# Kernel tuning notes

Hardware: AMD Instinct MI355X
Metric: run time of the kernel (lower is better)

## Reference

```python
import jax, jax.numpy as jnp
import numpy as np

NHEAD = 8
HB, WB = 16, 16  # block_size


def _mha(q, k, v, w_in, b_in, w_out, b_out, nhead):
    # q,k,v: [L, B, C] seq-first, like torch.nn.MultiheadAttention (eval mode, no dropout)
    Lq, B, C = q.shape
    d = C // nhead
    wq, wk, wv = jnp.split(w_in, 3, axis=0)
    bq, bk, bv = jnp.split(b_in, 3)
    qh = (q @ wq.T + bq).reshape(Lq, B, nhead, d).transpose(1, 2, 0, 3)        # [B,H,Lq,d]
    kh = (k @ wk.T + bk).reshape(k.shape[0], B, nhead, d).transpose(1, 2, 0, 3)
    vh = (v @ wv.T + bv).reshape(v.shape[0], B, nhead, d).transpose(1, 2, 0, 3)
    scale = 1.0 / jnp.sqrt(jnp.asarray(d, dtype=qh.dtype))
    scores = jnp.einsum('bhqd,bhkd->bhqk', qh * scale, kh)
    attn = jax.nn.softmax(scores, axis=-1)
    out = jnp.einsum('bhqk,bhkd->bhqd', attn, vh)                               # [B,H,Lq,d]
    out = out.transpose(2, 0, 1, 3).reshape(Lq, B, C)
    return out @ w_out.T + b_out


def setup_inputs() -> dict:
    key = jax.random.key(0)
    ks = jax.random.split(key, 12)
    n, c, t, h, w = 2, 256, 2, 64, 64
    q = jax.random.normal(ks[0], (n, c, t, h, w), dtype=jnp.float32)
    k = jax.random.normal(ks[1], (n, c, t, h, w), dtype=jnp.float32)
    v = jax.random.normal(ks[2], (n, c, t, h, w), dtype=jnp.float32)
    pos = jax.random.normal(ks[3], (n, c, t, h, w), dtype=jnp.float32)
    s = 0.02
    wl_in = jax.random.normal(ks[4], (3 * c, c), dtype=jnp.float32) * s
    bl_in = jnp.zeros((3 * c,), dtype=jnp.float32)
    wl_out = jax.random.normal(ks[5], (c, c), dtype=jnp.float32) * s
    bl_out = jnp.zeros((c,), dtype=jnp.float32)
    ws_in = jax.random.normal(ks[6], (3 * c, c), dtype=jnp.float32) * s
    bs_in = jnp.zeros((3 * c,), dtype=jnp.float32)
    ws_out = jax.random.normal(ks[7], (c, c), dtype=jnp.float32) * s
    bs_out = jnp.zeros((c,), dtype=jnp.float32)
    return {"q": q, "k": k, "v": v, "pos": pos,
            "wl_in": wl_in, "bl_in": bl_in, "wl_out": wl_out, "bl_out": bl_out,
            "ws_in": ws_in, "bs_in": bs_in, "ws_out": ws_out, "bs_out": bs_out}


def reference(q, k, v, pos, wl_in, bl_in, wl_out, bl_out, ws_in, bs_in, ws_out, bs_out):
    n, c, t_q, h, w = q.shape
    t_k = k.shape[2]
    bn_h, bn_w = h // HB, w // WB

    def to_long(x, t):
        # [n,c,t,h,w] -> [t*bn_h*bn_w, n*HB*WB, c]
        x = x.reshape(n, c, t, bn_h, HB, bn_w, WB).transpose(2, 3, 5, 0, 4, 6, 1)
        return x.reshape(t * bn_h * bn_w, n * HB * WB, c)

    ql = to_long(q, t_q)
    kl = to_long(k, t_k)
    vl = to_long(v, t_k)
    pl = to_long(pos, t_q)

    v1 = _mha(ql + pl, kl + pl, vl, wl_in, bl_in, wl_out, bl_out, NHEAD)

    def long_to_short(x):
        # [t*bn_h*bn_w, n*HB*WB, c] -> [t*HB*WB, n*bn_h*bn_w, c]
        x = x.reshape(t_q, bn_h, bn_w, n, HB, WB, c).transpose(0, 4, 5, 3, 1, 2, 6)
        return x.reshape(t_q * HB * WB, n * bn_h * bn_w, c)

    v2 = long_to_short(v1)
    ps = long_to_short(pl)

    out = _mha(v2 + ps, v2 + ps, v2, ws_in, bs_in, ws_out, bs_out, NHEAD)
    out = out.reshape(t_q, HB, WB, n, bn_h, bn_w, c).transpose(3, 6, 0, 4, 1, 5, 2)
    return out.reshape(n, c, t_q, h, w)
```

## Files before the change

### kernel.cpp

```cpp
#include <hip/hip_runtime.h>
#include <math.h>


#define SCALE_D32 0.17677669529663687f
#define EXP2_SCALE 0.25508680987930193f
#define GLOBAL_AS __attribute__((address_space(1)))
#define LDS_AS __attribute__((address_space(3)))

typedef short short8 __attribute__((ext_vector_type(8)));
typedef short short4v __attribute__((ext_vector_type(4)));
typedef short short2v __attribute__((ext_vector_type(2)));
typedef float floatx4 __attribute__((ext_vector_type(4)));

__device__ __forceinline__ short f2bf(float f) {
  union { float f; unsigned u; } x;
  x.f = f;
  unsigned r = x.u + 0x7fffu + ((x.u >> 16) & 1u);
  return (short)(r >> 16);
}
__device__ __forceinline__ float bf2f(short s) {
  union { unsigned u; float f; } x;
  x.u = ((unsigned)(unsigned short)s) << 16;
  return x.f;
}

__device__ __forceinline__ int o1s_phys(int q, int ch) {
  return q * 256 + (ch & ~63) + ((((ch >> 3) & 7) ^ (q & 7)) << 3) + (ch & 7);
}

__device__ __forceinline__ void stage_w(short* Wsl, const short* Wg, int kb,
                                        int wave, int lane, int rsub, int csub) {
#pragma unroll
  for (int j = 0; j < 8; ++j) {
    int r0 = (wave * 8 + j) * 8;
    int row = r0 + rsub;
    int c = csub ^ (row & 7);
    const short* gp = Wg + (long)row * 256 + kb * 64 + c * 8;
    short* lp = &Wsl[r0 * 64 + lane * 8];
    __builtin_amdgcn_global_load_lds((const GLOBAL_AS void*)gp,
                                     (LDS_AS void*)lp, 16, 0, 0);
  }
}

__device__ __forceinline__ void gemm_direct(
    const short* A, const short* Wg, floatx4 (&acc)[2][4],
    int wave, int l15, int quad, int x7) {
  const short* wrow = Wg + (wave * 64 + l15) * 256 + quad * 8;
  short8 bcur[4], bnxt[4];
#pragma unroll
  for (int nt = 0; nt < 4; ++nt)
    bcur[nt] = *(const short8*)(wrow + nt * 16 * 256);
#pragma unroll
  for (int t = 0; t < 8; ++t) {
    if (t < 7) {
#pragma unroll
      for (int nt = 0; nt < 4; ++nt)
        bnxt[nt] = *(const short8*)(wrow + nt * 16 * 256 + (t + 1) * 32);
    }
    int pcA = ((t & 1) * 4 + quad) ^ x7;
    short8 af[2];
#pragma unroll
    for (int mt = 0; mt < 2; ++mt)
      af[mt] = *(const short8*)&A[(mt * 16 + l15) * 256 + (t >> 1) * 64 + pcA * 8];
#pragma unroll
    for (int mt = 0; mt < 2; ++mt)
#pragma unroll
      for (int nt = 0; nt < 4; ++nt)
        acc[mt][nt] = __builtin_amdgcn_mfma_f32_16x16x32_bf16(
            af[mt], bcur[nt], acc[mt][nt], 0, 0, 0);
    if (t < 7) {
#pragma unroll
      for (int nt = 0; nt < 4; ++nt) bcur[nt] = bnxt[nt];
    }
  }
}

__device__ __forceinline__ void stage_tile(short* dst, const short* Xg,
                                           int b1, int tid) {
#pragma unroll
  for (int p = 0; p < 4; ++p) {
    int idx = p * 256 + tid;
    int row = idx >> 5;
    int ch = idx & 31;
    int chs = (ch & ~7) | ((ch & 7) ^ (row & 7));
    const short* gp = Xg + ((long)(row * 512 + b1)) * 256 + chs * 8;
    short* lp = dst + idx * 8;
    __builtin_amdgcn_global_load_lds((const GLOBAL_AS void*)gp,
                                     (LDS_AS void*)lp, 16, 0, 0);
  }
}

__global__ __launch_bounds__(256) void pack_kernel(
    const float* __restrict__ q, const float* __restrict__ k,
    const float* __restrict__ v, const float* __restrict__ pos,
    short* __restrict__ Xp, short* __restrict__ Xq,
    short* __restrict__ Xk, short* __restrict__ Xv,
    const float* __restrict__ wl_in, const float* __restrict__ wl_out,
    const float* __restrict__ ws_in, const float* __restrict__ ws_out,
    short* __restrict__ wbf) {
  __shared__ float tP[64][65];
  __shared__ float tX[64][65];
  int b = blockIdx.x;
  int cb = b & 3;
  int h  = (b >> 2) & 63;
  int nt = b >> 8;
  int n = nt >> 1, t = nt & 1;
  int c0 = cb * 64;
  int bh = h >> 4, ii = h & 15;
  long inbase = (long)n * 2097152 + (long)t * 4096 + (long)h * 64;
  int tx = threadIdx.x & 63;
  int ty = threadIdx.x >> 6;

  for (int cc = ty; cc < 64; cc += 4) {
    long a = inbase + (long)(c0 + cc) * 8192 + tx;
    tP[cc][tx] = pos[a];
    tX[cc][tx] = q[a];
  }
  __syncthreads();
  for (int ww = ty; ww < 64; ww += 4) {
    int bw = ww >> 4, j = ww & 15;
    int m1 = (((t * 4 + bh) * 4 + bw) * 512) + n * 256 + ii * 16 + j;
    long o = (long)m1 * 256 + c0 + tx;
    float pv = tP[tx][ww];
    Xp[o] = f2bf(pv);
    Xq[o] = f2bf(tX[tx][ww] + pv);
  }
  __syncthreads();
  for (int cc = ty; cc < 64; cc += 4) {
    long a = inbase + (long)(c0 + cc) * 8192 + tx;
    tX[cc][tx] = k[a];
  }
  __syncthreads();
  for (int ww = ty; ww < 64; ww += 4) {
    int bw = ww >> 4, j = ww & 15;
    int m1 = (((t * 4 + bh) * 4 + bw) * 512) + n * 256 + ii * 16 + j;
    long o = (long)m1 * 256 + c0 + tx;
    Xk[o] = f2bf(tX[tx][ww] + tP[tx][ww]);
  }
  __syncthreads();
  for (int cc = ty; cc < 64; cc += 4) {
    long a = inbase + (long)(c0 + cc) * 8192 + tx;
    tX[cc][tx] = v[a];
  }
  __syncthreads();
  for (int ww = ty; ww < 64; ww += 4) {
    int bw = ww >> 4, j = ww & 15;
    int m1 = (((t * 4 + bh) * 4 + bw) * 512) + n * 256 + ii * 16 + j;
    long o = (long)m1 * 256 + c0 + tx;
    Xv[o] = f2bf(tX[tx][ww]);
  }
  int idx = (blockIdx.x * 256 + threadIdx.x) * 2;
  const float* wp;
  if (idx < 196608) wp = wl_in + idx;
  else if (idx < 262144) wp = wl_out + (idx - 196608);
  else if (idx < 458752) wp = ws_in + (idx - 262144);
  else wp = ws_out + (idx - 458752);
  float2 wv = *(const float2*)wp;
  wbf[idx] = f2bf(wv.x);
  wbf[idx + 1] = f2bf(wv.y);
}

template <bool OUT32>
__global__ __launch_bounds__(256) void gemm_tri(
    const short* __restrict__ A0, const short* __restrict__ A1,
    const short* __restrict__ A2, const short* __restrict__ W0,
    const float* __restrict__ bias0, void* __restrict__ C0,
    void* __restrict__ C1, void* __restrict__ C2) {
  __shared__ short As[128 * 64];
  __shared__ short Ws[64 * 64];
  int z = blockIdx.z;
  const short* A = (z == 0) ? A0 : ((z == 1) ? A1 : A2);
  const short* Wb = W0 + z * 65536;
  const float* bias = bias0 + z * 256;
  void* Csel = (z == 0) ? C0 : ((z == 1) ? C1 : C2);
  int m0 = blockIdx.x * 128;
  int n0 = blockIdx.y * 64;
  int tid = threadIdx.x;
  int lane = tid & 63, wave = tid >> 6;
  int wm = wave >> 1, wn = wave & 1;
  int l15 = lane & 15, quad = lane >> 4;
  int x7 = l15 & 7;
  int rsub = lane >> 3;
  int csub = lane & 7;

  floatx4 acc[4][2];
#pragma unroll
  for (int mt = 0; mt < 4; ++mt)
#pragma unroll
    for (int nt = 0; nt < 2; ++nt) acc[mt][nt] = (floatx4)(0.f);

  for (int kb = 0; kb < 4; ++kb) {
    int k0 = kb * 64;
    if (kb) __syncthreads();
#pragma unroll
    for (int j = 0; j < 4; ++j) {
      int r0 = (wave * 4 + j) * 8;
      int row = r0 + rsub;
      int c = csub ^ (row & 7);
      const short* gp = A + (long)(m0 + row) * 256 + k0 + c * 8;
      short* lp = &As[r0 * 64 + lane * 8];
      __builtin_amdgcn_global_load_lds((const GLOBAL_AS void*)gp,
                                       (LDS_AS void*)lp, 16, 0, 0);
    }
#pragma unroll
    for (int j = 0; j < 2; ++j) {
      int r0 = (wave * 2 + j) * 8;
      int row = r0 + rsub;
      int c = csub ^ (row & 7);
      const short* gp = Wb + (long)(n0 + row) * 256 + k0 + c * 8;
      short* lp = &Ws[r0 * 64 + lane * 8];
      __builtin_amdgcn_global_load_lds((const GLOBAL_AS void*)gp,
                                       (LDS_AS void*)lp, 16, 0, 0);
    }
    __syncthreads();
#pragma unroll
    for (int ks = 0; ks < 2; ++ks) {
      int pc = (ks * 4 + quad) ^ x7;
      short8 af[4], bfr[2];
#pragma unroll
      for (int mt = 0; mt < 4; ++mt) {
        int row = wm * 64 + mt * 16 + l15;
        af[mt] = *(const short8*)&As[row * 64 + pc * 8];
      }
#pragma unroll
      for (int nt = 0; nt < 2; ++nt) {
        int row = wn * 32 + nt * 16 + l15;
        bfr[nt] = *(const short8*)&Ws[row * 64 + pc * 8];
      }
#pragma unroll
      for (int mt = 0; mt < 4; ++mt)
#pragma unroll
        for (int nt = 0; nt < 2; ++nt)
          acc[mt][nt] = __builtin_amdgcn_mfma_f32_16x16x32_bf16(
              af[mt], bfr[nt], acc[mt][nt], 0, 0, 0);
    }
  }
  float bia0 = bias[n0 + wn * 32 + l15];
  float bia1 = bias[n0 + wn * 32 + 16 + l15];
#pragma unroll
  for (int mt = 0; mt < 4; ++mt) {
#pragma unroll
    for (int r = 0; r < 4; ++r) {
      int row = m0 + wm * 64 + mt * 16 + quad * 4 + r;
      long base = (long)row * 256 + n0 + wn * 32 + l15;
      if (OUT32) {
        float* C = (float*)Csel;
        C[base] = acc[mt][0][r] + bia0;
        C[base + 16] = acc[mt][1][r] + bia1;
      } else {
        short* C = (short*)Csel;
        C[base] = f2bf(acc[mt][0][r] + bia0);
        C[base + 16] = f2bf(acc[mt][1][r] + bia1);
      }
    }
  }
}

__global__ __launch_bounds__(256) void attn1_giga(
    const short* __restrict__ Xq, const short* __restrict__ Xk,
    const short* __restrict__ Xv, const short* __restrict__ Xp,
    const short* __restrict__ Wlin, const float* __restrict__ bias_lin,
    const short* __restrict__ Wo, const float* __restrict__ bias_o,
    const short* __restrict__ Wsin, const float* __restrict__ bias_sin,
    short* __restrict__ Q2, short* __restrict__ K2, short* __restrict__ V2) {
  __shared__ short R1[32 * 256];
  __shared__ short R2[32 * 256];
  __shared__ short R3[32 * 256];
  __shared__ short R4[10240];
  int b1 = blockIdx.x;
  int tid = threadIdx.x;
  int wave = tid >> 6, lane = tid & 63;
  int l15 = lane & 15, quad = lane >> 4;
  int x7 = l15 & 7;

  stage_tile(R1, Xq, b1, tid);
  stage_tile(R2, Xk, b1, tid);
  stage_tile(R3, Xv, b1, tid);
  __syncthreads();

  floatx4 acc[2][4];

#pragma unroll 1
  for (int z = 0; z < 3; ++z) {
    short* Rz = (z == 0) ? R1 : ((z == 1) ? R2 : R3);
    const short* Wz = Wlin + z * 65536;
#pragma unroll
    for (int mt = 0; mt < 2; ++mt)
#pragma unroll
      for (int nt = 0; nt < 4; ++nt) acc[mt][nt] = (floatx4)(0.f);
    gemm_direct(Rz, Wz, acc, wave, l15, quad, x7);
    __syncthreads();
    float bz[4];
#pragma unroll
    for (int nt = 0; nt < 4; ++nt)
      bz[nt] = bias_lin[z * 256 + wave * 64 + nt * 16 + l15];
#pragma unroll
    for (int mt = 0; mt < 2; ++mt)
#pragma unroll
      for (int r = 0; r < 4; ++r) {
        int row = mt * 16 + quad * 4 + r;
#pragma unroll
        for (int nt = 0; nt < 4; ++nt) {
          int col = wave * 64 + nt * 16 + l15;
          Rz[o1s_phys(row, col)] = f2bf(acc[mt][nt][r] + bz[nt]);
        }
      }
  }
  __syncthreads();

  short* Vtb = R4;
  short* Pwb = R4 + 5120;
  int key = lane & 31;
  int dh = (lane >> 5) * 16;
  int pc2 = 2 * (key & 15) + (key >> 4);

  floatx4 oacc[2][4];
  float lsum[2][2][4];

#pragma unroll
  for (int h2 = 0; h2 < 2; ++h2) {
    int hh = wave * 2 + h2;
    int cb0 = hh * 32 + quad * 8;
    short8 qf0 = *(const short8*)&R1[o1s_phys(l15, cb0)];
    short8 qf1 = *(const short8*)&R1[o1s_phys(l15 + 16, cb0)];
    short8 kf0 = *(const short8*)&R2[o1s_phys(l15, cb0)];
    short8 kf1 = *(const short8*)&R2[o1s_phys(l15 + 16, cb0)];
    short8 v0 = *(const short8*)&R3[o1s_phys(key, hh * 32 + dh)];
    short8 v1 = *(const short8*)&R3[o1s_phys(key, hh * 32 + dh + 8)];
#pragma unroll
    for (int j = 0; j < 8; ++j) {
      Vtb[(wave * 32 + dh + j) * 40 + pc2] = v0[j];
      Vtb[(wave * 32 + dh + 8 + j) * 40 + pc2] = v1[j];
    }
    floatx4 s00 = __builtin_amdgcn_mfma_f32_16x16x32_bf16(qf0, kf0, (floatx4)(0.f), 0, 0, 0);
    floatx4 s01 = __builtin_amdgcn_mfma_f32_16x16x32_bf16(qf0, kf1, (floatx4)(0.f), 0, 0, 0);
    floatx4 s10 = __builtin_amdgcn_mfma_f32_16x16x32_bf16(qf1, kf0, (floatx4)(0.f), 0, 0, 0);
    floatx4 s11 = __builtin_amdgcn_mfma_f32_16x16x32_bf16(qf1, kf1, (floatx4)(0.f), 0, 0, 0);
    float li0[4], li1[4];
#pragma unroll
    for (int r = 0; r < 4; ++r) {
      float p00 = __builtin_amdgcn_exp2f(s00[r] * EXP2_SCALE);
      float p01 = __builtin_amdgcn_exp2f(s01[r] * EXP2_SCALE);
      float p10 = __builtin_amdgcn_exp2f(s10[r] * EXP2_SCALE);
      float p11 = __builtin_amdgcn_exp2f(s11[r] * EXP2_SCALE);
      li0[r] = p00 + p01;
      li1[r] = p10 + p11;
      short2v pa, pb;
      pa.x = f2bf(p00); pa.y = f2bf(p01);
      pb.x = f2bf(p10); pb.y = f2bf(p11);
      *(short2v*)&Pwb[(wave * 32 + quad * 4 + r) * 40 + 2 * l15] = pa;
      *(short2v*)&Pwb[(wave * 32 + 16 + quad * 4 + r) * 40 + 2 * l15] = pb;
    }
#pragma unroll
    for (int r = 0; r < 4; ++r) {
      li0[r] += __shfl_xor(li0[r], 1, 64);
      li0[r] += __shfl_xor(li0[r], 2, 64);
      li0[r] += __shfl_xor(li0[r], 4, 64);
      li0[r] += __shfl_xor(li0[r], 8, 64);
      li1[r] += __shfl_xor(li1[r], 1, 64);
      li1[r] += __shfl_xor(li1[r], 2, 64);
      li1[r] += __shfl_xor(li1[r], 4, 64);
      li1[r] += __shfl_xor(li1[r], 8, 64);
      lsum[h2][0][r] = li0[r];
      lsum[h2][1][r] = li1[r];
    }
    short8 pf0 = *(const short8*)&Pwb[(wave * 32 + l15) * 40 + quad * 8];
    short8 pf1 = *(const short8*)&Pwb[(wave * 32 + 16 + l15) * 40 + quad * 8];
    short8 vt0 = *(const short8*)&Vtb[(wave * 32 + l15) * 40 + quad * 8];
    short8 vt1 = *(const short8*)&Vtb[(wave * 32 + 16 + l15) * 40 + quad * 8];
    oacc[h2][0] = __builtin_amdgcn_mfma_f32_16x16x32_bf16(pf0, vt0, (floatx4)(0.f), 0, 0, 0);
    oacc[h2][1] = __builtin_amdgcn_mfma_f32_16x16x32_bf16(pf0, vt1, (floatx4)(0.f), 0, 0, 0);
    oacc[h2][2] = __builtin_amdgcn_mfma_f32_16x16x32_bf16(pf1, vt0, (floatx4)(0.f), 0, 0, 0);
    oacc[h2][3] = __builtin_amdgcn_mfma_f32_16x16x32_bf16(pf1, vt1, (floatx4)(0.f), 0, 0, 0);
  }

  __syncthreads();

#pragma unroll
  for (int h2 = 0; h2 < 2; ++h2) {
    int hh = wave * 2 + h2;
    int cA = hh * 32 + l15;
    int cB = cA + 16;
#pragma unroll
    for (int r = 0; r < 4; ++r) {
      float inv0 = 1.f / lsum[h2][0][r];
      float inv1 = 1.f / lsum[h2][1][r];
      int qa = quad * 4 + r, qb = 16 + quad * 4 + r;
      R1[o1s_phys(qa, cA)] = f2bf(oacc[h2][0][r] * inv0);
      R1[o1s_phys(qa, cB)] = f2bf(oacc[h2][1][r] * inv0);
      R1[o1s_phys(qb, cA)] = f2bf(oacc[h2][2][r] * inv1);
      R1[o1s_phys(qb, cB)] = f2bf(oacc[h2][3][r] * inv1);
    }
  }
  __syncthreads();

#pragma unroll
  for (int mt = 0; mt < 2; ++mt)
#pragma unroll
    for (int nt = 0; nt < 4; ++nt) acc[mt][nt] = (floatx4)(0.f);
  gemm_direct(R1, Wo, acc, wave, l15, quad, x7);

  {
    float bvo[4];
#pragma unroll
    for (int nt = 0; nt < 4; ++nt) bvo[nt] = bias_o[wave * 64 + nt * 16 + l15];
#pragma unroll
    for (int mt = 0; mt < 2; ++mt) {
#pragma unroll
      for (int r = 0; r < 4; ++r) {
        int qrow = mt * 16 + quad * 4 + r;
        long pbase = ((long)qrow * 512 + b1) * 256;
#pragma unroll
        for (int nt = 0; nt < 4; ++nt) {
          int col = wave * 64 + nt * 16 + l15;
          float val = acc[mt][nt][r] + bvo[nt];
          int ph = o1s_phys(qrow, col);
          R3[ph] = f2bf(val);
          R2[ph] = f2bf(val + bf2f(Xp[pbase + col]));
        }
      }
    }
  }
  __syncthreads();

  int nn = b1 >> 8, ii = (b1 >> 4) & 15, jj = b1 & 15;
#pragma unroll 1
  for (int z = 0; z < 3; ++z) {
    const short* Wz = Wsin + z * 65536;
    const short* Ab = (z < 2) ? R2 : R3;
    short* outz = (z == 0) ? Q2 : ((z == 1) ? K2 : V2);
    float bz[4];
#pragma unroll
    for (int nt = 0; nt < 4; ++nt)
      bz[nt] = bias_sin[z * 256 + wave * 64 + nt * 16 + l15];
#pragma unroll
    for (int mt = 0; mt < 2; ++mt)
#pragma unroll
      for (int nt = 0; nt < 4; ++nt) acc[mt][nt] = (floatx4)(0.f);
    gemm_direct(Ab, Wz, acc, wave, l15, quad, x7);
#pragma unroll
    for (int mt = 0; mt < 2; ++mt) {
#pragma unroll
      for (int r = 0; r < 4; ++r) {
        int qrow = mt * 16 + quad * 4 + r;
        int t = qrow >> 4, bh = (qrow >> 2) & 3, bw = qrow & 3;
        int m2 = (t * 256 + ii * 16 + jj) * 32 + nn * 16 + bh * 4 + bw;
        long xbase = (long)m2 * 256;
#pragma unroll
        for (int nt = 0; nt < 4; ++nt) {
          int col = wave * 64 + nt * 16 + l15;
          outz[xbase + col] = f2bf(acc[mt][nt][r] + bz[nt]);
        }
      }
    }
  }
}

__global__ __launch_bounds__(256) void attn2_mfma(
    const short* __restrict__ Q2, const short* __restrict__ K2,
    const short* __restrict__ V2, short* __restrict__ O2) {
  __shared__ short Ks[64][40];
  __shared__ short Vt[32][72];
  __shared__ short Pw[4][16][72];
  int bid = blockIdx.x;
  int rest = bid & 255;
  int qblk = bid >> 8;
  int hh = 2 * (rest & 3) + (rest >> 7);
  int b2 = (rest >> 2) & 31;
  int tid = threadIdx.x;
  int wave = tid >> 6, lane = tid & 63;
  int l15 = lane & 15, quad = lane >> 4;

  short8 qf;
  {
    long tok = (long)(qblk * 64 + wave * 16 + l15) * 32 + b2;
    qf = *(const short8*)(Q2 + tok * 256 + hh * 32 + quad * 8);
  }
  floatx4 Oa = (floatx4)(0.f), Ob = (floatx4)(0.f);
  float li[4] = {0.f, 0.f, 0.f, 0.f};

  int skey = tid >> 2;
  int sd0 = (tid & 3) * 8;
  int vkey = lane;
  int vd0 = wave * 8;
  int vcol = (vkey & 15) * 4 + (vkey >> 4);

  for (int kb = 0; kb < 8; ++kb) {
    if (kb) __syncthreads();
    {
      long tok = (long)(kb * 64 + skey) * 32 + b2;
      *(short8*)&Ks[skey][sd0] = *(const short8*)(K2 + tok * 256 + hh * 32 + sd0);
    }
    {
      long tok = (long)(kb * 64 + vkey) * 32 + b2;
      short8 v = *(const short8*)(V2 + tok * 256 + hh * 32 + vd0);
#pragma unroll
      for (int j = 0; j < 8; ++j) Vt[vd0 + j][vcol] = v[j];
    }
    __syncthreads();
    floatx4 st[4];
#pragma unroll
    for (int kt = 0; kt < 4; ++kt) {
      short8 kf = *(const short8*)&Ks[kt * 16 + l15][quad * 8];
      st[kt] = __builtin_amdgcn_mfma_f32_16x16x32_bf16(qf, kf, (floatx4)(0.f), 0, 0, 0);
    }
#pragma unroll
    for (int r = 0; r < 4; ++r) {
      float p0 = __builtin_amdgcn_exp2f(st[0][r] * EXP2_SCALE);
      float p1 = __builtin_amdgcn_exp2f(st[1][r] * EXP2_SCALE);
      float p2 = __builtin_amdgcn_exp2f(st[2][r] * EXP2_SCALE);
      float p3 = __builtin_amdgcn_exp2f(st[3][r] * EXP2_SCALE);
      li[r] += (p0 + p1) + (p2 + p3);
      short4v pp;
      pp.x = f2bf(p0); pp.y = f2bf(p1); pp.z = f2bf(p2); pp.w = f2bf(p3);
      *(short4v*)&Pw[wave][quad * 4 + r][l15 * 4] = pp;
    }
#pragma unroll
    for (int kk = 0; kk < 2; ++kk) {
      short8 pf = *(const short8*)&Pw[wave][l15][kk * 32 + quad * 8];
      short8 v0 = *(const short8*)&Vt[l15][kk * 32 + quad * 8];
      short8 v1 = *(const short8*)&Vt[16 + l15][kk * 32 + quad * 8];
      Oa = __builtin_amdgcn_mfma_f32_16x16x32_bf16(pf, v0, Oa, 0, 0, 0);
      Ob = __builtin_amdgcn_mfma_f32_16x16x32_bf16(pf, v1, Ob, 0, 0, 0);
    }
  }
#pragma unroll
  for (int r = 0; r < 4; ++r) {
    float s = li[r];
    s += __shfl_xor(s, 1, 64);
    s += __shfl_xor(s, 2, 64);
    s += __shfl_xor(s, 4, 64);
    s += __shfl_xor(s, 8, 64);
    float inv = 1.f / s;
    long tok = (long)(qblk * 64 + wave * 16 + quad * 4 + r) * 32 + b2;
    long a = tok * 256 + hh * 32 + l15;
    O2[a] = f2bf(Oa[r] * inv);
    O2[a + 16] = f2bf(Ob[r] * inv);
  }
}

__global__ __launch_bounds__(256) void unpack_kernel(
    const float* __restrict__ Y, float* __restrict__ out) {
  __shared__ float tl[64][65];
  int b = blockIdx.x;
  int cb = b & 3;
  int h = (b >> 2) & 63;
  int nt = b >> 8;
  int n = nt >> 1, t = nt & 1;
  int c0 = cb * 64;
  int bh = h >> 4, ii = h & 15;
  int tx = threadIdx.x & 63;
  int ty = threadIdx.x >> 6;
  for (int ww = ty; ww < 64; ww += 4) {
    int bw = ww >> 4, j = ww & 15;
    int l2 = t * 256 + ii * 16 + j;
    int b2 = n * 16 + bh * 4 + bw;
    int m2 = l2 * 32 + b2;
    tl[tx][ww] = Y[(long)m2 * 256 + c0 + tx];
  }
  __syncthreads();
  long ob = (long)n * 2097152 + (long)t * 4096 + (long)h * 64 + tx;
  for (int cc = ty; cc < 64; cc += 4) {
    out[ob + (long)(c0 + cc) * 8192] = tl[cc][tx];
  }
}

extern "C" void kernel_launch(void* const* d_in, const int* in_sizes, int n_in,
                              void* d_out, int out_size, void* d_ws, size_t ws_size,
                              hipStream_t stream) {
  const float* q      = (const float*)d_in[0];
  const float* k      = (const float*)d_in[1];
  const float* v      = (const float*)d_in[2];
  const float* pos    = (const float*)d_in[3];
  const float* wl_in  = (const float*)d_in[4];
  const float* bl_in  = (const float*)d_in[5];
  const float* wl_out = (const float*)d_in[6];
  const float* bl_out = (const float*)d_in[7];
  const float* ws_in  = (const float*)d_in[8];
  const float* bs_in  = (const float*)d_in[9];
  const float* ws_out = (const float*)d_in[10];
  const float* bs_out = (const float*)d_in[11];
  float* out = (float*)d_out;
  char* wsb = (char*)d_ws;
  const size_t SLB = 16777216;
  short* s0 = (short*)(wsb);
  short* wbf = (short*)(wsb + SLB / 2);
  short* s1 = (short*)(wsb + SLB);
  short* s2 = (short*)(wsb + 2 * SLB);
  short* s3 = (short*)(wsb + 3 * SLB);
  short* s4 = (short*)(wsb + 4 * SLB);
  short* s5 = (short*)(wsb + 5 * SLB);
  short* s6 = (short*)(wsb + 6 * SLB);

  pack_kernel<<<1024, 256, 0, stream>>>(q, k, v, pos, s0, s1, s2, s3,
                                        wl_in, wl_out, ws_in, ws_out, wbf);

  attn1_giga<<<512, 256, 0, stream>>>(s1, s2, s3, s0, wbf, bl_in,
                                      wbf + 196608, bl_out,
                                      wbf + 262144, bs_in, s4, s5, s6);

  attn2_mfma<<<2048, 256, 0, stream>>>(s4, s5, s6, s1);
  dim3 g1(128, 4, 1);
  gemm_tri<true><<<g1, 256, 0, stream>>>(s1, s1, s1, wbf + 458752, bs_out,
                                         s2, s2, s2);

  unpack_kernel<<<1024, 256, 0, stream>>>((const float*)s2, out);
}
```

Baseline: 223.4 us.

## Pair two attention tiles per block and share weight slabs through LDS

The fused attention/projection kernel now runs 512 threads handling two 32-row tiles per block. The 256x256 weight matrices are staged into LDS in 64-column slabs and shared by both groups, instead of each wave reading weights directly from global memory. This halves global weight traffic per tile and removes some barriers. In exchange it adds a sync pair per K-slab, uses more LDS (which lowers occupancy), and cuts the grid to 256 blocks. Several __syncthreads were dropped where the new gemm's internal barriers now order the phases.

```diff
diff --git a/kernel.cpp b/kernel.cpp
--- a/kernel.cpp
+++ b/kernel.cpp
@@ -28,65 +28,44 @@
   return q * 256 + (ch & ~63) + ((((ch >> 3) & 7) ^ (q & 7)) << 3) + (ch & 7);
 }
 
-__device__ __forceinline__ void stage_w(short* Wsl, const short* Wg, int kb,
-                                        int wave, int lane, int rsub, int csub) {
-#pragma unroll
-  for (int j = 0; j < 8; ++j) {
-    int r0 = (wave * 8 + j) * 8;
-    int row = r0 + rsub;
-    int c = csub ^ (row & 7);
-    const short* gp = Wg + (long)row * 256 + kb * 64 + c * 8;
-    short* lp = &Wsl[r0 * 64 + lane * 8];
+__device__ __forceinline__ void stage_w512(short* Ws, const short* Wg,
+                                           int kb, int tid) {
+#pragma unroll
+  for (int j = 0; j < 4; ++j) {
+    int idx = j * 512 + tid;
+    int row = idx >> 3;
+    int c = idx & 7;
+    int cs = c ^ (row & 7);
+    const short* gp = Wg + (long)row * 256 + kb * 64 + cs * 8;
     __builtin_amdgcn_global_load_lds((const GLOBAL_AS void*)gp,
-                                     (LDS_AS void*)lp, 16, 0, 0);
-  }
-}
-
-__device__ __forceinline__ void gemm_direct(
-    const short* A, const short* Wg, floatx4 (&acc)[2][4],
-    int wave, int l15, int quad, int x7) {
-  const short* wrow = Wg + (wave * 64 + l15) * 256 + quad * 8;
-  short8 bcur[4], bnxt[4];
-#pragma unroll
-  for (int nt = 0; nt < 4; ++nt)
-    bcur[nt] = *(const short8*)(wrow + nt * 16 * 256);
-#pragma unroll
-  for (int t = 0; t < 8; ++t) {
-    if (t < 7) {
+                                     (LDS_AS void*)(Ws + idx * 8), 16, 0, 0);
+  }
+}
+
+__device__ __forceinline__ void gemm_shared(
+    const short* A, const short* Wg, short* Ws, floatx4 (&acc)[2][4],
+    int tid, int wv, int l15, int quad, int x7) {
+  for (int kb = 0; kb < 4; ++kb) {
+    __syncthreads();
+    stage_w512(Ws, Wg, kb, tid);
+    __syncthreads();
+#pragma unroll
+    for (int ks = 0; ks < 2; ++ks) {
+      int pc = (ks * 4 + quad) ^ x7;
+      short8 af[2], bfr[4];
+#pragma unroll
+      for (int mt = 0; mt < 2; ++mt)
+        af[mt] = *(const short8*)&A[(mt * 16 + l15) * 256 + kb * 64 + pc * 8];
 #pragma unroll
       for (int nt = 0; nt < 4; ++nt)
-        bnxt[nt] = *(const short8*)(wrow + nt * 16 * 256 + (t + 1) * 32);
-    }
-    int pcA = ((t & 1) * 4 + quad) ^ x7;
-    short8 af[2];
-#pragma unroll
-    for (int mt = 0; mt < 2; ++mt)
-      af[mt] = *(const short8*)&A[(mt * 16 + l15) * 256 + (t >> 1) * 64 + pcA * 8];
-#pragma unroll
-    for (int mt = 0; mt < 2; ++mt)
-#pragma unroll
-      for (int nt = 0; nt < 4; ++nt)
-        acc[mt][nt] = __builtin_amdgcn_mfma_f32_16x16x32_bf16(
-            af[mt], bcur[nt], acc[mt][nt], 0, 0, 0);
-    if (t < 7) {
-#pragma unroll
-      for (int nt = 0; nt < 4; ++nt) bcur[nt] = bnxt[nt];
-    }
-  }
-}
-
-__device__ __forceinline__ void stage_tile(short* dst, const short* Xg,
-                                           int b1, int tid) {
-#pragma unroll
-  for (int p = 0; p < 4; ++p) {
-    int idx = p * 256 + tid;
-    int row = idx >> 5;
-    int ch = idx & 31;
-    int chs = (ch & ~7) | ((ch & 7) ^ (row & 7));
-    const short* gp = Xg + ((long)(row * 512 + b1)) * 256 + chs * 8;
-    short* lp = dst + idx * 8;
-    __builtin_amdgcn_global_load_lds((const GLOBAL_AS void*)gp,
-                                     (LDS_AS void*)lp, 16, 0, 0);
+        bfr[nt] = *(const short8*)&Ws[(wv * 64 + nt * 16 + l15) * 64 + pc * 8];
+#pragma unroll
+      for (int mt = 0; mt < 2; ++mt)
+#pragma unroll
+        for (int nt = 0; nt < 4; ++nt)
+          acc[mt][nt] = __builtin_amdgcn_mfma_f32_16x16x32_bf16(
+              af[mt], bfr[nt], acc[mt][nt], 0, 0, 0);
+    }
   }
 }
 
@@ -256,26 +235,40 @@
   }
 }
 
-__global__ __launch_bounds__(256) void attn1_giga(
+__global__ __launch_bounds__(512, 2) void attn1_giga(
     const short* __restrict__ Xq, const short* __restrict__ Xk,
     const short* __restrict__ Xv, const short* __restrict__ Xp,
     const short* __restrict__ Wlin, const float* __restrict__ bias_lin,
     const short* __restrict__ Wo, const float* __restrict__ bias_o,
     const short* __restrict__ Wsin, const float* __restrict__ bias_sin,
     short* __restrict__ Q2, short* __restrict__ K2, short* __restrict__ V2) {
-  __shared__ short R1[32 * 256];
-  __shared__ short R2[32 * 256];
-  __shared__ short R3[32 * 256];
-  __shared__ short R4[10240];
-  int b1 = blockIdx.x;
+  __shared__ short TILES[6 * 8192];
+  __shared__ short R4[20480];
   int tid = threadIdx.x;
   int wave = tid >> 6, lane = tid & 63;
+  int g = wave >> 2, wv = wave & 3;
+  int b1 = blockIdx.x * 2 + g;
   int l15 = lane & 15, quad = lane >> 4;
   int x7 = l15 & 7;
-
-  stage_tile(R1, Xq, b1, tid);
-  stage_tile(R2, Xk, b1, tid);
-  stage_tile(R3, Xv, b1, tid);
+  short* Ws = R4;
+  short* R1 = TILES + g * 24576;
+  short* R2 = R1 + 8192;
+  short* R3 = R1 + 16384;
+
+#pragma unroll
+  for (int p = 0; p < 12; ++p) {
+    const int tz = p >> 1;
+    const int gs = tz / 3, z = tz % 3;
+    int local = (p & 1) * 512 + tid;
+    int row = local >> 5, ch = local & 31;
+    int chs = (ch & ~7) | ((ch & 7) ^ (row & 7));
+    const short* Xg = (z == 0) ? Xq : ((z == 1) ? Xk : Xv);
+    const short* gp =
+        Xg + ((long)(row * 512 + blockIdx.x * 2 + gs)) * 256 + chs * 8;
+    __builtin_amdgcn_global_load_lds(
+        (const GLOBAL_AS void*)gp,
+        (LDS_AS void*)(TILES + tz * 8192 + local * 8), 16, 0, 0);
+  }
   __syncthreads();
 
   floatx4 acc[2][4];
@@ -288,12 +281,12 @@
     for (int mt = 0; mt < 2; ++mt)
 #pragma unroll
       for (int nt = 0; nt < 4; ++nt) acc[mt][nt] = (floatx4)(0.f);
-    gemm_direct(Rz, Wz, acc, wave, l15, quad, x7);
+    gemm_shared(Rz, Wz, Ws, acc, tid, wv, l15, quad, x7);
     __syncthreads();
     float bz[4];
 #pragma unroll
     for (int nt = 0; nt < 4; ++nt)
-      bz[nt] = bias_lin[z * 256 + wave * 64 + nt * 16 + l15];
+      bz[nt] = bias_lin[z * 256 + wv * 64 + nt * 16 + l15];
 #pragma unroll
     for (int mt = 0; mt < 2; ++mt)
 #pragma unroll
@@ -301,7 +294,7 @@
         int row = mt * 16 + quad * 4 + r;
 #pragma unroll
         for (int nt = 0; nt < 4; ++nt) {
-          int col = wave * 64 + nt * 16 + l15;
+          int col = wv * 64 + nt * 16 + l15;
           Rz[o1s_phys(row, col)] = f2bf(acc[mt][nt][r] + bz[nt]);
         }
       }
@@ -309,7 +302,7 @@
   __syncthreads();
 
   short* Vtb = R4;
-  short* Pwb = R4 + 5120;
+  short* Pwb = R4 + 10240;
   int key = lane & 31;
   int dh = (lane >> 5) * 16;
   int pc2 = 2 * (key & 15) + (key >> 4);
@@ -319,7 +312,7 @@
 
 #pragma unroll
   for (int h2 = 0; h2 < 2; ++h2) {
-    int hh = wave * 2 + h2;
+    int hh = wv * 2 + h2;
     int cb0 = hh * 32 + quad * 8;
     short8 qf0 = *(const short8*)&R1[o1s_phys(l15, cb0)];
     short8 qf1 = *(const short8*)&R1[o1s_phys(l15 + 16, cb0)];
@@ -374,11 +367,9 @@
     oacc[h2][3] = __builtin_amdgcn_mfma_f32_16x16x32_bf16(pf1, vt1, (floatx4)(0.f), 0, 0, 0);
   }
 
-  __syncthreads();
-
 #pragma unroll
   for (int h2 = 0; h2 < 2; ++h2) {
-    int hh = wave * 2 + h2;
+    int hh = wv * 2 + h2;
     int cA = hh * 32 + l15;
     int cB = cA + 16;
 #pragma unroll
@@ -392,18 +383,17 @@
       R1[o1s_phys(qb, cB)] = f2bf(oacc[h2][3][r] * inv1);
     }
   }
-  __syncthreads();
 
 #pragma unroll
   for (int mt = 0; mt < 2; ++mt)
 #pragma unroll
     for (int nt = 0; nt < 4; ++nt) acc[mt][nt] = (floatx4)(0.f);
-  gemm_direct(R1, Wo, acc, wave, l15, quad, x7);
+  gemm_shared(R1, Wo, Ws, acc, tid, wv, l15, quad, x7);
 
   {
     float bvo[4];
 #pragma unroll
-    for (int nt = 0; nt < 4; ++nt) bvo[nt] = bias_o[wave * 64 + nt * 16 + l15];
+    for (int nt = 0; nt < 4; ++nt) bvo[nt] = bias_o[wv * 64 + nt * 16 + l15];
 #pragma unroll
     for (int mt = 0; mt < 2; ++mt) {
 #pragma unroll
@@ -412,7 +402,7 @@
         long pbase = ((long)qrow * 512 + b1) * 256;
 #pragma unroll
         for (int nt = 0; nt < 4; ++nt) {
-          int col = wave * 64 + nt * 16 + l15;
+          int col = wv * 64 + nt * 16 + l15;
           float val = acc[mt][nt][r] + bvo[nt];
           int ph = o1s_phys(qrow, col);
           R3[ph] = f2bf(val);
@@ -421,7 +411,6 @@
       }
     }
   }
-  __syncthreads();
 
   int nn = b1 >> 8, ii = (b1 >> 4) & 15, jj = b1 & 15;
 #pragma unroll 1
@@ -432,12 +421,12 @@
     float bz[4];
 #pragma unroll
     for (int nt = 0; nt < 4; ++nt)
-      bz[nt] = bias_sin[z * 256 + wave * 64 + nt * 16 + l15];
+      bz[nt] = bias_sin[z * 256 + wv * 64 + nt * 16 + l15];
 #pragma unroll
     for (int mt = 0; mt < 2; ++mt)
 #pragma unroll
       for (int nt = 0; nt < 4; ++nt) acc[mt][nt] = (floatx4)(0.f);
-    gemm_direct(Ab, Wz, acc, wave, l15, quad, x7);
+    gemm_shared(Ab, Wz, Ws, acc, tid, wv, l15, quad, x7);
 #pragma unroll
     for (int mt = 0; mt < 2; ++mt) {
 #pragma unroll
@@ -448,7 +437,7 @@
         long xbase = (long)m2 * 256;
 #pragma unroll
         for (int nt = 0; nt < 4; ++nt) {
-          int col = wave * 64 + nt * 16 + l15;
+          int col = wv * 64 + nt * 16 + l15;
           outz[xbase + col] = f2bf(acc[mt][nt][r] + bz[nt]);
         }
       }
@@ -595,7 +584,7 @@
   pack_kernel<<<1024, 256, 0, stream>>>(q, k, v, pos, s0, s1, s2, s3,
                                         wl_in, wl_out, ws_in, ws_out, wbf);
 
-  attn1_giga<<<512, 256, 0, stream>>>(s1, s2, s3, s0, wbf, bl_in,
+  attn1_giga<<<256, 512, 0, stream>>>(s1, s2, s3, s0, wbf, bl_in,
                                       wbf + 196608, bl_out,
                                       wbf + 262144, bs_in, s4, s5, s6);
 
```

Result: faster. 204.4 us (-8.5%).
